# Optimization experiments

Hardware: AMD Instinct MI355X
Metric: run time of the kernel (lower is better)

Reference implementation:

```python
import jax, jax.numpy as jnp
import numpy as np

N, E, G = 50000, 600000, 512   # nodes, edges, graphs
F, D, L = 128, 128, 3          # in_features, hidden dim, num_gc_layers
ED = D * L                      # embedding_dim (readout='concat')
C = 1.0                         # curvature
MIN_NORM = 1e-15
BALL_EPS = 4e-3                 # hgcn PoincareBall proj eps for float32


def _logmap0(p, c):
    sc = jnp.sqrt(c)
    n = jnp.clip(jnp.linalg.norm(p, axis=-1, keepdims=True), MIN_NORM, None)
    return p / (sc * n) * jnp.arctanh(jnp.clip(sc * n, -1 + 1e-15, 1 - 1e-15))


def _expmap0(u, c):
    sc = jnp.sqrt(c)
    n = jnp.clip(jnp.linalg.norm(u, axis=-1, keepdims=True), MIN_NORM, None)
    return jnp.tanh(sc * n) * u / (sc * n)


def _proj(x, c):
    n = jnp.clip(jnp.linalg.norm(x, axis=-1, keepdims=True), MIN_NORM, None)
    maxn = (1.0 - BALL_EPS) / jnp.sqrt(c)
    return jnp.where(n > maxn, x / n * maxn, x)


def _gcn(x, W, b, src, dst):
    h = x @ W
    deg = jax.ops.segment_sum(jnp.ones_like(dst, dtype=h.dtype), dst, num_segments=N) + 1.0
    dinv = deg ** -0.5
    msg = h[src] * (dinv[src] * dinv[dst])[:, None]           # [E, D]
    agg = jax.ops.segment_sum(msg, dst, num_segments=N) + h * (dinv * dinv)[:, None]
    return agg + b


def _encoder(x, Ws, bs, src, dst, batch):
    xs = []
    for W, b in zip(Ws, bs):
        x = jax.nn.relu(_gcn(x, W, b, src, dst))
        xs.append(x)
    # readout='concat' with global_add_pool
    g = jnp.concatenate([jax.ops.segment_sum(h, batch, num_segments=G) for h in xs], axis=1)
    return g, jnp.concatenate(xs, axis=1)


def _mlp(x, W1, W2):  # proj_head: Linear (no bias), ReLU, Linear (no bias)
    return jax.nn.relu(x @ W1) @ W2


def setup_inputs() -> dict:
    key = jax.random.key(0)
    ks = jax.random.split(key, 24)

    def xav(k, i, o):
        return jax.random.normal(k, (i, o), dtype=jnp.float32) * np.float32(np.sqrt(2.0 / (i + o)))

    inp = {
        'x':   jax.random.normal(ks[0], (N, F), dtype=jnp.float32) * 1e-3,  # points inside the ball
        'x_s': jax.random.normal(ks[1], (N, F), dtype=jnp.float32) * 1e-3,
        'src': jax.random.randint(ks[2], (E,), 0, N, dtype=jnp.int32),
        'dst': jax.random.randint(ks[3], (E,), 0, N, dtype=jnp.int32),
        'batch': jnp.sort(jax.random.randint(ks[4], (N,), 0, G, dtype=jnp.int32)),
        # feature-branch GCN encoder
        'Wf0': xav(ks[5], F, D), 'Wf1': xav(ks[6], D, D), 'Wf2': xav(ks[7], D, D),
        'bf0': jnp.zeros((D,), jnp.float32), 'bf1': jnp.zeros((D,), jnp.float32), 'bf2': jnp.zeros((D,), jnp.float32),
        # structure-branch GCN encoder
        'Ws0': xav(ks[8], F, D), 'Ws1': xav(ks[9], D, D), 'Ws2': xav(ks[10], D, D),
        'bs0': jnp.zeros((D,), jnp.float32), 'bs1': jnp.zeros((D,), jnp.float32), 'bs2': jnp.zeros((D,), jnp.float32),
        # proj heads (biases removed by init_emb)
        'P1': xav(ks[11], ED, ED), 'P2': xav(ks[12], ED, ED),
        'G1': xav(ks[13], 2 * ED, ED), 'G2': xav(ks[14], ED, ED),
    }
    return inp


def reference(x, x_s, Wf0, Wf1, Wf2, bf0, bf1, bf2, Ws0, Ws1, Ws2, bs0, bs1, bs2, P1, P2, G1, G2, src, dst, batch):
    xt_f = _logmap0(x, C)
    xt_s = _logmap0(x_s, C)
    g_f, n_f = _encoder(xt_f, (Wf0, Wf1, Wf2), (bf0, bf1, bf2), src, dst, batch)
    g_s, n_s = _encoder(xt_s, (Ws0, Ws1, Ws2), (bs0, bs1, bs2), src, dst, batch)
    g = _mlp(jnp.concatenate((g_f, g_s), axis=1), G1, G2)
    e = lambda t: _proj(_expmap0(t, C), C)
    return (e(g), e(_mlp(g_f, P1, P2)), e(_mlp(n_f, P1, P2)), e(_mlp(g_s, P1, P2)), e(_mlp(n_s, P1, P2)))
```

## Files before the change

### kernel.cpp

```cpp
#include <hip/hip_runtime.h>
#include <math.h>

#define N_NODES 50000
#define N_EDGES 600000
#define N_GRAPHS 512
#define F_IN 128
#define D_HID 128
#define EDIM 384
#define M_ALL (N_NODES + N_GRAPHS)

typedef __attribute__((ext_vector_type(8))) short bf16x8;
typedef __attribute__((ext_vector_type(4))) float f32x4;
typedef __attribute__((ext_vector_type(16))) float f32x16;

static __device__ __forceinline__ float wave_reduce_sum(float s) {
#pragma unroll
  for (int off = 32; off > 0; off >>= 1) s += __shfl_xor(s, off, 64);
  return s;
}

static __device__ __forceinline__ int wave_reduce_sum_i(int s) {
#pragma unroll
  for (int off = 32; off > 0; off >>= 1) s += __shfl_xor(s, off, 64);
  return s;
}

static __device__ __forceinline__ short f2b(float f) {
  unsigned u = __float_as_uint(f);
  unsigned r = (u + 0x7FFFu + ((u >> 16) & 1u)) >> 16;
  return (short)r;
}

static __device__ __forceinline__ float b2f(short s) {
  return __uint_as_float(((unsigned)(unsigned short)s) << 16);
}


#define SCAN_BS 256
#define SCAN_NB ((N_NODES + SCAN_BS - 1) / SCAN_BS)

__global__ __launch_bounds__(SCAN_BS) void init_kernel(const int* __restrict__ batch,
                                                       int* __restrict__ cnt,
                                                       int* __restrict__ gptr) {
  int i = blockIdx.x * SCAN_BS + threadIdx.x;
  if (i < N_NODES) cnt[i] = 0;
  if (i <= N_GRAPHS) {
    int lo = 0, hi = N_NODES;
    while (lo < hi) { int mid = (lo + hi) >> 1; if (batch[mid] < i) lo = mid + 1; else hi = mid; }
    gptr[i] = lo;
  }
}

__global__ void hist_kernel(const int* __restrict__ dst, int* __restrict__ cnt) {
  int i = blockIdx.x * blockDim.x + threadIdx.x;
  if (i < N_EDGES) atomicAdd(&cnt[dst[i]], 1);
}

__global__ __launch_bounds__(SCAN_BS) void scan1_kernel(const int* __restrict__ cnt,
                                                        int* __restrict__ row_ptr,
                                                        int* __restrict__ bsum) {
  __shared__ int wsum[4];
  int tid = threadIdx.x, lane = tid & 63, wid = tid >> 6;
  int idx = blockIdx.x * SCAN_BS + tid;
  int v = (idx < N_NODES) ? cnt[idx] : 0;
  int x = v;
#pragma unroll
  for (int off = 1; off < 64; off <<= 1) {
    int t = __shfl_up(x, off, 64);
    if (lane >= off) x += t;
  }
  if (lane == 63) wsum[wid] = x;
  __syncthreads();
  int pre = 0, tot = 0;
#pragma unroll
  for (int w = 0; w < 4; ++w) { int s = wsum[w]; tot += s; if (w < wid) pre += s; }
  if (idx < N_NODES) row_ptr[idx + 1] = x + pre;
  if (tid == 0) bsum[blockIdx.x] = tot;
}

__global__ __launch_bounds__(SCAN_BS) void scan3_kernel(const int* __restrict__ cnt,
                                                        const int* __restrict__ bsum,
                                                        int* __restrict__ row_ptr,
                                                        int* __restrict__ cursor,
                                                        float* __restrict__ dinv) {
  __shared__ int ws[4];
  int tid = threadIdx.x, lane = tid & 63, wid = tid >> 6;
  int v = 0;
  if (tid < SCAN_NB && tid < blockIdx.x) v = bsum[tid];
  v = wave_reduce_sum_i(v);
  if (lane == 0) ws[wid] = v;
  __syncthreads();
  int boff = ws[0] + ws[1] + ws[2] + ws[3];
  int idx = blockIdx.x * SCAN_BS + tid;
  if (idx >= N_NODES) return;
  int val = row_ptr[idx + 1] + boff;
  row_ptr[idx + 1] = val;
  int c = cnt[idx];
  cursor[idx] = val - c;
  dinv[idx] = 1.0f / sqrtf((float)(c + 1));
  if (idx == 0) row_ptr[0] = 0;
}

__global__ void scatter_kernel(const int* __restrict__ src, const int* __restrict__ dst,
                               const float* __restrict__ dinv, int* __restrict__ cursor,
                               int* __restrict__ col, float* __restrict__ ew) {
  int e = blockIdx.x * blockDim.x + threadIdx.x;
  if (e >= N_EDGES) return;
  int s = src[e], d = dst[e];
  int pos = atomicAdd(&cursor[d], 1);
  col[pos] = s;
  ew[pos] = dinv[s] * dinv[d];
}


struct WcSeg { const float* W; short* Wt; int K; int Nc; };
struct WcArgs { WcSeg seg[10]; };

__global__ void wconv_all_kernel(WcArgs a) {
  int sidx = blockIdx.y;
  WcSeg s = a.seg[sidx];
  int i = blockIdx.x * blockDim.x + threadIdx.x;
  if (i >= s.K * s.Nc) return;
  int k = i / s.Nc, n = i - k * s.Nc;
  s.Wt[(size_t)n * s.K + k] = f2b(s.W[i]);
}


__global__ __launch_bounds__(256) void logmap2_kernel(const float* __restrict__ x,
                                                      const float* __restrict__ x_s,
                                                      short* __restrict__ Ab) {
  int w = blockIdx.x * 4 + (threadIdx.x >> 6);
  int lane = threadIdx.x & 63;
  if (w >= 2 * N_NODES) return;
  int br = (w >= N_NODES) ? 1 : 0;
  int row = br ? (w - N_NODES) : w;
  const float* xr = (br ? x_s : x) + (size_t)row * F_IN;
  float2 v = *(const float2*)(xr + lane * 2);
  float s = wave_reduce_sum(v.x * v.x + v.y * v.y);
  float n = sqrtf(s);
  float nc = fmaxf(n, 1e-15f);
  float f = atanhf(fminf(nc, 0.9999999f)) / nc;
  short2 o; o.x = f2b(v.x * f); o.y = f2b(v.y * f);
  *(short2*)(Ab + (size_t)row * 256 + br * 128 + lane * 2) = o;
}


__global__ __launch_bounds__(256) void agg2_kernel(const short* __restrict__ Xin, int lda,
                                                   const float* __restrict__ dinv,
                                                   const int* __restrict__ row_ptr,
                                                   const int* __restrict__ col,
                                                   const float* __restrict__ ew,
                                                   short* __restrict__ Xa) {
  int node = blockIdx.x * 4 + (threadIdx.x >> 6);
  int lane = threadIdx.x & 63;
  if (node >= N_NODES) return;
  float di = dinv[node];
  float wsf = di * di;
  short4 sv = *(const short4*)(Xin + (size_t)node * lda + lane * 4);
  float a0 = b2f(sv.x) * wsf, a1 = b2f(sv.y) * wsf, a2 = b2f(sv.z) * wsf, a3 = b2f(sv.w) * wsf;
  int s = row_ptr[node], e = row_ptr[node + 1];
  int j = s;
  for (; j + 4 <= e; j += 4) {
    int c0 = col[j], c1 = col[j + 1], c2 = col[j + 2], c3 = col[j + 3];
    float w0 = ew[j], w1 = ew[j + 1], w2 = ew[j + 2], w3 = ew[j + 3];
    short4 v0 = *(const short4*)(Xin + (size_t)c0 * lda + lane * 4);
    short4 v1 = *(const short4*)(Xin + (size_t)c1 * lda + lane * 4);
    short4 v2 = *(const short4*)(Xin + (size_t)c2 * lda + lane * 4);
    short4 v3 = *(const short4*)(Xin + (size_t)c3 * lda + lane * 4);
    a0 += b2f(v0.x) * w0; a1 += b2f(v0.y) * w0; a2 += b2f(v0.z) * w0; a3 += b2f(v0.w) * w0;
    a0 += b2f(v1.x) * w1; a1 += b2f(v1.y) * w1; a2 += b2f(v1.z) * w1; a3 += b2f(v1.w) * w1;
    a0 += b2f(v2.x) * w2; a1 += b2f(v2.y) * w2; a2 += b2f(v2.z) * w2; a3 += b2f(v2.w) * w2;
    a0 += b2f(v3.x) * w3; a1 += b2f(v3.y) * w3; a2 += b2f(v3.z) * w3; a3 += b2f(v3.w) * w3;
  }
  for (; j < e; ++j) {
    float w0 = ew[j];
    short4 v0 = *(const short4*)(Xin + (size_t)col[j] * lda + lane * 4);
    a0 += b2f(v0.x) * w0; a1 += b2f(v0.y) * w0; a2 += b2f(v0.z) * w0; a3 += b2f(v0.w) * w0;
  }
  short4 o; o.x = f2b(a0); o.y = f2b(a1); o.z = f2b(a2); o.w = f2b(a3);
  *(short4*)(Xa + (size_t)node * 256 + lane * 4) = o;
}


#define LDK 40

struct GemmZArgs {
  const short* A[2];
  const short* Bt[2];
  const float* bias[2];
  short* Cb[2];
  int lda, ldc, M, Nc, K, kexp, do_relu;
};

__global__ __launch_bounds__(256) void mfma_gemmz_kernel(GemmZArgs g) {
  __shared__ __align__(16) short As[128 * LDK];
  __shared__ __align__(16) short Bs[128 * LDK];
  int z = blockIdx.z;
  const short* __restrict__ A = g.A[z];
  const short* __restrict__ Bt = g.Bt[z];
  int tid = threadIdx.x;
  int wave = tid >> 6, lane = tid & 63;
  int wr = (wave >> 1) * 64, wc = (wave & 1) * 64;
  int q = lane >> 4, m = lane & 15;
  int row0 = blockIdx.x * 128, col0 = blockIdx.y * 128;
  f32x4 acc[4][4] = {};
  for (int k0 = 0; k0 < g.K; k0 += 32) {
#pragma unroll
    for (int p = 0; p < 2; ++p) {
      int idx = p * 256 + tid;
      int r = idx >> 2, kc = (idx & 3) * 8;
      int gr = row0 + r;
      int kk = k0 + kc;
      int acol = g.kexp ? (kk + ((kk >> 7) << 7)) : kk;
      float4 v = make_float4(0.f, 0.f, 0.f, 0.f);
      if (gr < g.M) v = *(const float4*)(A + (size_t)gr * g.lda + acol);
      *(float4*)(As + r * LDK + kc) = v;
      float4 w = *(const float4*)(Bt + (size_t)(col0 + r) * g.K + kk);
      *(float4*)(Bs + r * LDK + kc) = w;
    }
    __syncthreads();
    bf16x8 af[4], bfr[4];
#pragma unroll
    for (int i = 0; i < 4; ++i) {
      af[i]  = *(const bf16x8*)(As + (wr + i * 16 + m) * LDK + q * 8);
      bfr[i] = *(const bf16x8*)(Bs + (wc + i * 16 + m) * LDK + q * 8);
    }
#pragma unroll
    for (int i = 0; i < 4; ++i)
#pragma unroll
      for (int j = 0; j < 4; ++j)
        acc[i][j] = __builtin_amdgcn_mfma_f32_16x16x32_bf16(af[i], bfr[j], acc[i][j], 0, 0, 0);
    __syncthreads();
  }
  const float* __restrict__ bias = g.bias[z];
  short* __restrict__ Cb = g.Cb[z];
#pragma unroll
  for (int i = 0; i < 4; ++i) {
#pragma unroll
    for (int r = 0; r < 4; ++r) {
      int rr = row0 + wr + i * 16 + q * 4 + r;
      if (rr >= g.M) continue;
#pragma unroll
      for (int j = 0; j < 4; ++j) {
        int cc = col0 + wc + j * 16 + m;
        float v = acc[i][j][r];
        if (bias) v += bias[cc];
        if (g.do_relu) v = fmaxf(v, 0.0f);
        Cb[(size_t)rr * g.ldc + cc] = f2b(v);
      }
    }
  }
}


#define HLD 392

struct MlpProb {
  const short* A;
  const short* B1;
  const short* B2;
  float* Cf;
  float* Cf2;
  int lda, M, K1, kexp, split;
};
struct Mlp2Args { MlpProb p[3]; int gx_h; };

__global__ __launch_bounds__(512) void mlp2_kernel(Mlp2Args g) {
  __shared__ __align__(16) short As[128 * LDK];
  __shared__ __align__(16) short Bs[384 * LDK];
  __shared__ __align__(16) short H[128 * HLD];
  __shared__ float nsum[128][4];
  int z = blockIdx.z;
  int bx = blockIdx.x;
  MlpProb p;
  int row0;
  if (bx < g.gx_h) { p = g.p[z]; row0 = bx * 128; }
  else { if (z) return; p = g.p[2]; row0 = (bx - g.gx_h) * 128; }

  int tid = threadIdx.x;
  int wave = tid >> 6, lane = tid & 63;
  int l31 = lane & 31, lh = lane >> 5;
  int rg = wave & 1;
  int cq = wave >> 1;

  f32x16 acc[2][3] = {};
  for (int k0 = 0; k0 < p.K1; k0 += 32) {
    {
      int r = tid >> 2, kc = (tid & 3) * 8;
      int gr = row0 + r;
      int kk = k0 + kc;
      int acol = p.kexp ? (kk + ((kk >> 7) << 7)) : kk;
      float4 v = make_float4(0.f, 0.f, 0.f, 0.f);
      if (gr < p.M) v = *(const float4*)(p.A + (size_t)gr * p.lda + acol);
      *(float4*)(As + r * LDK + kc) = v;
    }
#pragma unroll
    for (int q = 0; q < 3; ++q) {
      int idx = q * 512 + tid;
      int r = idx >> 2, kc = (idx & 3) * 8;
      float4 w0 = *(const float4*)(p.B1 + (size_t)r * p.K1 + k0 + kc);
      *(float4*)(Bs + r * LDK + kc) = w0;
    }
    __syncthreads();
#pragma unroll
    for (int ks = 0; ks < 32; ks += 16) {
      int kloc = ks + lh * 8;
      bf16x8 a0 = *(const bf16x8*)(As + (rg * 64 + l31) * LDK + kloc);
      bf16x8 a1 = *(const bf16x8*)(As + (rg * 64 + 32 + l31) * LDK + kloc);
      bf16x8 b0 = *(const bf16x8*)(Bs + (cq * 96 + l31) * LDK + kloc);
      bf16x8 b1 = *(const bf16x8*)(Bs + (cq * 96 + 32 + l31) * LDK + kloc);
      bf16x8 b2 = *(const bf16x8*)(Bs + (cq * 96 + 64 + l31) * LDK + kloc);
      acc[0][0] = __builtin_amdgcn_mfma_f32_32x32x16_bf16(a0, b0, acc[0][0], 0, 0, 0);
      acc[1][0] = __builtin_amdgcn_mfma_f32_32x32x16_bf16(a1, b0, acc[1][0], 0, 0, 0);
      acc[0][1] = __builtin_amdgcn_mfma_f32_32x32x16_bf16(a0, b1, acc[0][1], 0, 0, 0);
      acc[1][1] = __builtin_amdgcn_mfma_f32_32x32x16_bf16(a1, b1, acc[1][1], 0, 0, 0);
      acc[0][2] = __builtin_amdgcn_mfma_f32_32x32x16_bf16(a0, b2, acc[0][2], 0, 0, 0);
      acc[1][2] = __builtin_amdgcn_mfma_f32_32x32x16_bf16(a1, b2, acc[1][2], 0, 0, 0);
    }
    __syncthreads();
  }
#pragma unroll
  for (int rf = 0; rf < 2; ++rf)
#pragma unroll
    for (int f = 0; f < 3; ++f)
#pragma unroll
      for (int reg = 0; reg < 16; ++reg) {
        int rl = rg * 64 + rf * 32 + (reg & 3) + 8 * (reg >> 2) + 4 * lh;
        H[rl * HLD + cq * 96 + f * 32 + l31] = f2b(fmaxf(acc[rf][f][reg], 0.0f));
      }
#pragma unroll
  for (int rf = 0; rf < 2; ++rf)
#pragma unroll
    for (int f = 0; f < 3; ++f) acc[rf][f] = (f32x16){};
  __syncthreads();
  for (int k0 = 0; k0 < 384; k0 += 32) {
#pragma unroll
    for (int q = 0; q < 3; ++q) {
      int idx = q * 512 + tid;
      int r = idx >> 2, kc = (idx & 3) * 8;
      float4 w0 = *(const float4*)(p.B2 + (size_t)r * 384 + k0 + kc);
      *(float4*)(Bs + r * LDK + kc) = w0;
    }
    __syncthreads();
#pragma unroll
    for (int ks = 0; ks < 32; ks += 16) {
      int kloc = ks + lh * 8;
      bf16x8 a0 = *(const bf16x8*)(H + (rg * 64 + l31) * HLD + k0 + kloc);
      bf16x8 a1 = *(const bf16x8*)(H + (rg * 64 + 32 + l31) * HLD + k0 + kloc);
      bf16x8 b0 = *(const bf16x8*)(Bs + (cq * 96 + l31) * LDK + kloc);
      bf16x8 b1 = *(const bf16x8*)(Bs + (cq * 96 + 32 + l31) * LDK + kloc);
      bf16x8 b2 = *(const bf16x8*)(Bs + (cq * 96 + 64 + l31) * LDK + kloc);
      acc[0][0] = __builtin_amdgcn_mfma_f32_32x32x16_bf16(a0, b0, acc[0][0], 0, 0, 0);
      acc[1][0] = __builtin_amdgcn_mfma_f32_32x32x16_bf16(a1, b0, acc[1][0], 0, 0, 0);
      acc[0][1] = __builtin_amdgcn_mfma_f32_32x32x16_bf16(a0, b1, acc[0][1], 0, 0, 0);
      acc[1][1] = __builtin_amdgcn_mfma_f32_32x32x16_bf16(a1, b1, acc[1][1], 0, 0, 0);
      acc[0][2] = __builtin_amdgcn_mfma_f32_32x32x16_bf16(a0, b2, acc[0][2], 0, 0, 0);
      acc[1][2] = __builtin_amdgcn_mfma_f32_32x32x16_bf16(a1, b2, acc[1][2], 0, 0, 0);
    }
    __syncthreads();
  }
#pragma unroll
  for (int rf = 0; rf < 2; ++rf)
#pragma unroll
    for (int reg = 0; reg < 16; ++reg) {
      float s = acc[rf][0][reg] * acc[rf][0][reg] + acc[rf][1][reg] * acc[rf][1][reg] +
                acc[rf][2][reg] * acc[rf][2][reg];
      s += __shfl_xor(s, 1, 64);
      s += __shfl_xor(s, 2, 64);
      s += __shfl_xor(s, 4, 64);
      s += __shfl_xor(s, 8, 64);
      s += __shfl_xor(s, 16, 64);
      if (l31 == 0)
        nsum[rg * 64 + rf * 32 + (reg & 3) + 8 * (reg >> 2) + 4 * lh][cq] = s;
    }
  __syncthreads();
  const float maxn = 1.0f - 4e-3f;
#pragma unroll
  for (int rf = 0; rf < 2; ++rf)
#pragma unroll
    for (int reg = 0; reg < 16; ++reg) {
      int rl = rg * 64 + rf * 32 + (reg & 3) + 8 * (reg >> 2) + 4 * lh;
      int rr = row0 + rl;
      if (rr >= p.M) continue;
      float s = nsum[rl][0] + nsum[rl][1] + nsum[rl][2] + nsum[rl][3];
      float n = fmaxf(sqrtf(s), 1e-15f);
      float th = tanhf(n);
      float fct = th / n;
      float n2 = fmaxf(th, 1e-15f);
      if (n2 > maxn) fct *= maxn / n2;
      float* base = (rr < p.split) ? (p.Cf + (size_t)rr * 384)
                                   : (p.Cf2 + (size_t)(rr - p.split) * 384);
#pragma unroll
      for (int f = 0; f < 3; ++f)
        base[cq * 96 + f * 32 + l31] = acc[rf][f][reg] * fct;
    }
}


__global__ __launch_bounds__(768) void pool2_kernel(const short* __restrict__ NB,
                                                    const int* __restrict__ gptr,
                                                    short* __restrict__ GCb,
                                                    short* __restrict__ nbappend) {
  int g = blockIdx.x, t = threadIdx.x;
  int s = gptr[g], e = gptr[g + 1];
  float acc = 0.0f;
  for (int i = s; i < e; ++i) acc += b2f(NB[(size_t)i * 768 + t]);
  short bv = f2b(acc);
  int l = t >> 8, rem = t & 255, b = rem >> 7, c = rem & 127;
  GCb[(size_t)g * 768 + b * 384 + l * 128 + c] = bv;
  nbappend[(size_t)g * 768 + t] = bv;
}


extern "C" void kernel_launch(void* const* d_in, const int* in_sizes, int n_in,
                              void* d_out, int out_size, void* d_ws, size_t ws_size,
                              hipStream_t stream) {
  (void)in_sizes; (void)n_in; (void)out_size; (void)ws_size;
  const float* x   = (const float*)d_in[0];
  const float* x_s = (const float*)d_in[1];
  const int* src   = (const int*)d_in[2];
  const int* dst   = (const int*)d_in[3];
  const int* batch = (const int*)d_in[4];
  const float* Wf[3] = {(const float*)d_in[5], (const float*)d_in[6], (const float*)d_in[7]};
  const float* bf[3] = {(const float*)d_in[8], (const float*)d_in[9], (const float*)d_in[10]};
  const float* Wsb[3] = {(const float*)d_in[11], (const float*)d_in[12], (const float*)d_in[13]};
  const float* bs[3] = {(const float*)d_in[14], (const float*)d_in[15], (const float*)d_in[16]};
  const float* P1 = (const float*)d_in[17];
  const float* P2 = (const float*)d_in[18];
  const float* G1 = (const float*)d_in[19];
  const float* G2 = (const float*)d_in[20];
  float* out = (float*)d_out;

  char* w = (char*)d_ws;
  auto alloc = [&](size_t bytes) {
    char* p = w;
    w += (bytes + 255) & ~(size_t)255;
    return p;
  };
  short* Ab    = (short*)alloc((size_t)N_NODES * 256 * 2);
  short* Xa    = (short*)alloc((size_t)N_NODES * 256 * 2);
  short* NB    = (short*)alloc((size_t)M_ALL * 768 * 2);
  int* cnt     = (int*)alloc((size_t)N_NODES * 4);
  int* row_ptr = (int*)alloc((size_t)(N_NODES + 1) * 4);
  int* cursor  = (int*)alloc((size_t)N_NODES * 4);
  float* dinv  = (float*)alloc((size_t)N_NODES * 4);
  int* col     = (int*)alloc((size_t)N_EDGES * 4);
  float* ew    = (float*)alloc((size_t)N_EDGES * 4);
  int* gptr    = (int*)alloc((size_t)(N_GRAPHS + 1) * 4);
  int* bsum    = (int*)alloc(256 * 4);
  short* GCb   = (short*)alloc((size_t)N_GRAPHS * 768 * 2);
  short* P1t   = (short*)alloc((size_t)EDIM * EDIM * 2);
  short* P2t   = (short*)alloc((size_t)EDIM * EDIM * 2);
  short* G1t   = (short*)alloc((size_t)768 * EDIM * 2);
  short* G2t   = (short*)alloc((size_t)EDIM * EDIM * 2);
  short* Wft[3], *Wst[3];
  for (int l = 0; l < 3; ++l) {
    Wft[l] = (short*)alloc((size_t)128 * 128 * 2);
    Wst[l] = (short*)alloc((size_t)128 * 128 * 2);
  }

  {
    WcArgs wa;
    wa.seg[0] = {P1, P1t, EDIM, EDIM};
    wa.seg[1] = {P2, P2t, EDIM, EDIM};
    wa.seg[2] = {G1, G1t, 768, EDIM};
    wa.seg[3] = {G2, G2t, EDIM, EDIM};
    for (int l = 0; l < 3; ++l) {
      wa.seg[4 + l] = {Wf[l], Wft[l], 128, 128};
      wa.seg[7 + l] = {Wsb[l], Wst[l], 128, 128};
    }
    wconv_all_kernel<<<dim3((768 * EDIM + 255) / 256, 10), 256, 0, stream>>>(wa);
  }

  init_kernel<<<SCAN_NB, SCAN_BS, 0, stream>>>(batch, cnt, gptr);
  hist_kernel<<<(N_EDGES + 255) / 256, 256, 0, stream>>>(dst, cnt);
  scan1_kernel<<<SCAN_NB, SCAN_BS, 0, stream>>>(cnt, row_ptr, bsum);
  scan3_kernel<<<SCAN_NB, SCAN_BS, 0, stream>>>(cnt, bsum, row_ptr, cursor, dinv);
  scatter_kernel<<<(N_EDGES + 255) / 256, 256, 0, stream>>>(src, dst, dinv, cursor, col, ew);

  const size_t OUT0 = 0;
  const size_t OUT1 = (size_t)N_GRAPHS * EDIM;
  const size_t OUT2 = OUT1 + (size_t)N_GRAPHS * EDIM;
  const size_t OUT3 = OUT2 + (size_t)N_NODES * EDIM;

  const int gx_layer = (N_NODES + 127) / 128;
  const int gx_mfma  = (M_ALL + 127) / 128;
  const int gx_agg   = (N_NODES + 3) / 4;

  logmap2_kernel<<<(2 * N_NODES + 3) / 4, 256, 0, stream>>>(x, x_s, Ab);

  const short* cur = Ab;
  int clda = 256;
  for (int l = 0; l < 3; ++l) {
    agg2_kernel<<<gx_agg, 256, 0, stream>>>(cur, clda, dinv, row_ptr, col, ew, Xa);
    GemmZArgs ga = {};
    ga.A[0] = Xa;        ga.A[1] = Xa + 128;
    ga.Bt[0] = Wft[l];   ga.Bt[1] = Wst[l];
    ga.bias[0] = bf[l];  ga.bias[1] = bs[l];
    ga.Cb[0] = NB + l * 256;        ga.Cb[1] = NB + l * 256 + 128;
    ga.lda = 256; ga.ldc = 768; ga.M = N_NODES; ga.Nc = 128; ga.K = 128;
    ga.kexp = 0; ga.do_relu = 1;
    mfma_gemmz_kernel<<<dim3(gx_layer, 1, 2), 256, 0, stream>>>(ga);
    cur = NB + l * 256;
    clda = 768;
  }

  pool2_kernel<<<N_GRAPHS, 768, 0, stream>>>(NB, gptr, GCb, NB + (size_t)N_NODES * 768);

  {
    const int gx_g = (N_GRAPHS + 127) / 128;
    Mlp2Args h = {};
    h.p[0] = {NB,       P1t, P2t, out + OUT2,
              out + OUT1, 768, M_ALL, EDIM, 1, N_NODES};
    h.p[1] = {NB + 128, P1t, P2t, out + OUT3 + (size_t)N_GRAPHS * EDIM,
              out + OUT3, 768, M_ALL, EDIM, 1, N_NODES};
    h.p[2] = {GCb, G1t, G2t, out + OUT0, out + OUT0, 768, N_GRAPHS, 768, 0, 1 << 30};
    h.gx_h = gx_mfma;
    mlp2_kernel<<<dim3(gx_mfma + gx_g, 1, 2), 512, 0, stream>>>(h);
  }
}
```

Measured before the change: 748.7 us.

## Register-prefetch next K-tile in MLP kernel and use raw barriers

The two GEMM loops in the MLP head kernel now load the next K-slice of A and B into registers before the MFMA work on the current slice, and prefetch the first B2 tile during the last B1 iteration. Synchronisation switches from __syncthreads to s_barrier with explicit lgkmcnt waits, so global loads stay in flight across the barrier. This aims to hide global-load latency behind MFMA compute at the cost of extra registers. The trailing s_barrier without an lgkmcnt wait relies on LDS reads having completed before operands are consumed, which is the subtle point.

```diff
diff --git a/kernel.cpp b/kernel.cpp
--- a/kernel.cpp
+++ b/kernel.cpp
@@ -283,25 +283,43 @@
   int rg = wave & 1;
   int cq = wave >> 1;
 
+  int r_a = tid >> 2, kc_a = (tid & 3) * 8;
+
+  auto loadA1 = [&](int k0) {
+    int gr = row0 + r_a;
+    int kk = k0 + kc_a;
+    int acol = p.kexp ? (kk + ((kk >> 7) << 7)) : kk;
+    float4 v = make_float4(0.f, 0.f, 0.f, 0.f);
+    if (gr < p.M) v = *(const float4*)(p.A + (size_t)gr * p.lda + acol);
+    return v;
+  };
+
   f32x16 acc[2][3] = {};
+  float4 pa, pb0, pb1, pb2;
+  pa = loadA1(0);
+  pb0 = *(const float4*)(p.B1 + (size_t)(0 * 128 + r_a) * p.K1 + kc_a);
+  pb1 = *(const float4*)(p.B1 + (size_t)(1 * 128 + r_a) * p.K1 + kc_a);
+  pb2 = *(const float4*)(p.B1 + (size_t)(2 * 128 + r_a) * p.K1 + kc_a);
+
   for (int k0 = 0; k0 < p.K1; k0 += 32) {
-    {
-      int r = tid >> 2, kc = (tid & 3) * 8;
-      int gr = row0 + r;
-      int kk = k0 + kc;
-      int acol = p.kexp ? (kk + ((kk >> 7) << 7)) : kk;
-      float4 v = make_float4(0.f, 0.f, 0.f, 0.f);
-      if (gr < p.M) v = *(const float4*)(p.A + (size_t)gr * p.lda + acol);
-      *(float4*)(As + r * LDK + kc) = v;
-    }
-#pragma unroll
-    for (int q = 0; q < 3; ++q) {
-      int idx = q * 512 + tid;
-      int r = idx >> 2, kc = (idx & 3) * 8;
-      float4 w0 = *(const float4*)(p.B1 + (size_t)r * p.K1 + k0 + kc);
-      *(float4*)(Bs + r * LDK + kc) = w0;
-    }
-    __syncthreads();
+    *(float4*)(As + r_a * LDK + kc_a) = pa;
+    *(float4*)(Bs + (0 * 128 + r_a) * LDK + kc_a) = pb0;
+    *(float4*)(Bs + (1 * 128 + r_a) * LDK + kc_a) = pb1;
+    *(float4*)(Bs + (2 * 128 + r_a) * LDK + kc_a) = pb2;
+    int kn = k0 + 32;
+    if (kn < p.K1) {
+      pa = loadA1(kn);
+      pb0 = *(const float4*)(p.B1 + (size_t)(0 * 128 + r_a) * p.K1 + kn + kc_a);
+      pb1 = *(const float4*)(p.B1 + (size_t)(1 * 128 + r_a) * p.K1 + kn + kc_a);
+      pb2 = *(const float4*)(p.B1 + (size_t)(2 * 128 + r_a) * p.K1 + kn + kc_a);
+    } else {
+      pb0 = *(const float4*)(p.B2 + (size_t)(0 * 128 + r_a) * 384 + kc_a);
+      pb1 = *(const float4*)(p.B2 + (size_t)(1 * 128 + r_a) * 384 + kc_a);
+      pb2 = *(const float4*)(p.B2 + (size_t)(2 * 128 + r_a) * 384 + kc_a);
+    }
+    asm volatile("s_waitcnt lgkmcnt(0)" ::: "memory");
+    __builtin_amdgcn_sched_barrier(0);
+    __builtin_amdgcn_s_barrier();
 #pragma unroll
     for (int ks = 0; ks < 32; ks += 16) {
       int kloc = ks + lh * 8;
@@ -317,7 +335,7 @@
       acc[0][2] = __builtin_amdgcn_mfma_f32_32x32x16_bf16(a0, b2, acc[0][2], 0, 0, 0);
       acc[1][2] = __builtin_amdgcn_mfma_f32_32x32x16_bf16(a1, b2, acc[1][2], 0, 0, 0);
     }
-    __syncthreads();
+    __builtin_amdgcn_s_barrier();
   }
 #pragma unroll
   for (int rf = 0; rf < 2; ++rf)
@@ -332,16 +350,22 @@
   for (int rf = 0; rf < 2; ++rf)
 #pragma unroll
     for (int f = 0; f < 3; ++f) acc[rf][f] = (f32x16){};
-  __syncthreads();
+  asm volatile("s_waitcnt lgkmcnt(0)" ::: "memory");
+  __builtin_amdgcn_sched_barrier(0);
+  __builtin_amdgcn_s_barrier();
   for (int k0 = 0; k0 < 384; k0 += 32) {
-#pragma unroll
-    for (int q = 0; q < 3; ++q) {
-      int idx = q * 512 + tid;
-      int r = idx >> 2, kc = (idx & 3) * 8;
-      float4 w0 = *(const float4*)(p.B2 + (size_t)r * 384 + k0 + kc);
-      *(float4*)(Bs + r * LDK + kc) = w0;
-    }
-    __syncthreads();
+    *(float4*)(Bs + (0 * 128 + r_a) * LDK + kc_a) = pb0;
+    *(float4*)(Bs + (1 * 128 + r_a) * LDK + kc_a) = pb1;
+    *(float4*)(Bs + (2 * 128 + r_a) * LDK + kc_a) = pb2;
+    int kn = k0 + 32;
+    if (kn < 384) {
+      pb0 = *(const float4*)(p.B2 + (size_t)(0 * 128 + r_a) * 384 + kn + kc_a);
+      pb1 = *(const float4*)(p.B2 + (size_t)(1 * 128 + r_a) * 384 + kn + kc_a);
+      pb2 = *(const float4*)(p.B2 + (size_t)(2 * 128 + r_a) * 384 + kn + kc_a);
+    }
+    asm volatile("s_waitcnt lgkmcnt(0)" ::: "memory");
+    __builtin_amdgcn_sched_barrier(0);
+    __builtin_amdgcn_s_barrier();
 #pragma unroll
     for (int ks = 0; ks < 32; ks += 16) {
       int kloc = ks + lh * 8;
@@ -357,7 +381,7 @@
       acc[0][2] = __builtin_amdgcn_mfma_f32_32x32x16_bf16(a0, b2, acc[0][2], 0, 0, 0);
       acc[1][2] = __builtin_amdgcn_mfma_f32_32x32x16_bf16(a1, b2, acc[1][2], 0, 0, 0);
     }
-    __syncthreads();
+    __builtin_amdgcn_s_barrier();
   }
 #pragma unroll
   for (int rf = 0; rf < 2; ++rf)
```

Result: faster. 720.3 us, median of 2 (-3.8%).
